# Kernel optimization log

Hardware: AMD Instinct MI355X
Metric: run time of the kernel (lower is better)

Reference implementation:

```python
import jax, jax.numpy as jnp
import numpy as np

H = 64  # hidden_size, hard-coded in module


def _lstm_layer(xs, W_ih, W_hh, b_ih, b_hh):
    """Run one LSTM layer over time-major xs [T, B, D_in].
    PyTorch gate order: i, f, g, o. Returns (hs [T,B,H], h_last [B,H])."""
    T, B, _ = xs.shape
    b = b_ih + b_hh
    # Precompute input contribution for all timesteps: [T, B, 4H]
    x_gates = jnp.einsum('tbd,gd->tbg', xs, W_ih) + b

    def step(carry, xg_t):
        h, c = carry
        gates = xg_t + h @ W_hh.T  # [B, 4H]
        i, f, g, o = jnp.split(gates, 4, axis=-1)
        i = jax.nn.sigmoid(i)
        f = jax.nn.sigmoid(f)
        g = jnp.tanh(g)
        o = jax.nn.sigmoid(o)
        c = f * c + i * g
        h = o * jnp.tanh(c)
        return (h, c), h

    h0 = jnp.zeros((B, H), xs.dtype)
    c0 = jnp.zeros((B, H), xs.dtype)
    (h_last, _), hs = jax.lax.scan(step, (h0, c0), x_gates)
    return hs, h_last


def setup_inputs() -> dict:
    key = jax.random.key(0)
    ks = jax.random.split(key, 12)
    B, T, C_in, E = 256, 4000, 1, 128
    s0 = 1.0 / np.sqrt(H)  # PyTorch LSTM init scale
    inp = {
        'x': jax.random.normal(ks[0], (B, T, C_in), jnp.float32),
        'W_ih0': jax.random.uniform(ks[1], (4 * H, C_in), jnp.float32, -s0, s0),
        'W_hh0': jax.random.uniform(ks[2], (4 * H, H), jnp.float32, -s0, s0),
        'b_ih0': jax.random.uniform(ks[3], (4 * H,), jnp.float32, -s0, s0),
        'b_hh0': jax.random.uniform(ks[4], (4 * H,), jnp.float32, -s0, s0),
        'W_ih1': jax.random.uniform(ks[5], (4 * H, H), jnp.float32, -s0, s0),
        'W_hh1': jax.random.uniform(ks[6], (4 * H, H), jnp.float32, -s0, s0),
        'b_ih1': jax.random.uniform(ks[7], (4 * H,), jnp.float32, -s0, s0),
        'b_hh1': jax.random.uniform(ks[8], (4 * H,), jnp.float32, -s0, s0),
        'W_fc': jax.random.uniform(ks[9], (E, H), jnp.float32, -s0, s0),
        'b_fc': jax.random.uniform(ks[10], (E,), jnp.float32, -s0, s0),
    }
    return inp


def reference(x, W_ih0, W_hh0, b_ih0, b_hh0, W_ih1, W_hh1, b_ih1, b_hh1, W_fc, b_fc):
    # x: [B, T, 1] (batch_first) -> time-major [T, B, 1]
    xs = jnp.swapaxes(x.astype(jnp.float32), 0, 1)
    hs0, _ = _lstm_layer(xs, W_ih0, W_hh0, b_ih0, b_hh0)
    _, h_last = _lstm_layer(hs0, W_ih1, W_hh1, b_ih1, b_hh1)
    # fc on final hidden state of the last layer: [B, E]
    return h_last @ W_fc.T + b_fc
```

## Files before the change

kernel.cpp:

```cpp
#include <hip/hip_runtime.h>

#define TT 4000
#define HH 64
#define NB 256
#define EE 128

typedef __attribute__((ext_vector_type(2))) _Float16 h2;
typedef __attribute__((ext_vector_type(8))) _Float16 h8;

__device__ __forceinline__ float ftanh(float x) {
    return fmaf(2.f, __builtin_amdgcn_rcpf(1.f + __expf(-2.f * x)), -1.f);
}

#if __has_builtin(__builtin_amdgcn_fdot2)
#define FDOT2(a, b, c) __builtin_amdgcn_fdot2((a), (b), (c), false)
#else
#define FDOT2(a, b, c) fmaf((float)(a).x, (float)(b).x, fmaf((float)(a).y, (float)(b).y, (c)))
#endif

#define H2V(V, i) (__builtin_shufflevector((V), (V), 2 * (i), 2 * (i) + 1))

template <int CTRL>
__device__ __forceinline__ float dpp_mov(float v) {
    return __int_as_float(__builtin_amdgcn_update_dpp(
        0, __float_as_int(v), CTRL, 0xF, 0xF, true));
}
#define DPP_XOR1 0xB1
#define DPP_XOR2 0x4E
#define DPP_FB   0x44
#define DPP_OB   0xEE
#define DPP_SHR4 0x114

#define CVT2(d0, d1, s) h2 d0 = h2{(_Float16)(s).x, (_Float16)(s).y}, \
                           d1 = h2{(_Float16)(s).z, (_Float16)(s).w};

#define D4(acc, W0, W1, W2, W3, Hv) \
    acc = FDOT2(W0, H2V(Hv, 0), acc); \
    acc = FDOT2(W1, H2V(Hv, 1), acc); \
    acc = FDOT2(W2, H2V(Hv, 2), acc); \
    acc = FDOT2(W3, H2V(Hv, 3), acc);

__global__ __launch_bounds__(256, 1)
void lstm2_fc_kernel(const float* __restrict__ x,
                     const float* __restrict__ W_ih0,
                     const float* __restrict__ W_hh0,
                     const float* __restrict__ b_ih0,
                     const float* __restrict__ b_hh0,
                     const float* __restrict__ W_ih1,
                     const float* __restrict__ W_hh1,
                     const float* __restrict__ b_ih1,
                     const float* __restrict__ b_hh1,
                     const float* __restrict__ W_fc,
                     const float* __restrict__ b_fc,
                     float* __restrict__ out)
{
    const int b    = blockIdx.x;
    const int tid  = threadIdx.x;
    const int w    = tid >> 6;
    const int lane = tid & 63;
    const int ss   = lane & 1;
    const int uu   = (lane >> 1) & 1;
    const int pp   = (lane >> 2) & 1;
    const int nn   = (lane >> 3) & 1;
    const int na   = w * 8 + (lane >> 4) * 2 + nn;
    const int nb   = na + 32;
    const int gidx = pp + 2 * uu;

    __shared__ float x_s[TT];
    __shared__ __align__(16) _Float16 hbuf[2][2 * HH];

    for (int t = tid; t < TT; t += 256) x_s[t] = x[(size_t)b * TT + t];
    if (tid < 4 * HH) ((_Float16*)hbuf)[tid] = (_Float16)0.f;

    const int rowa = gidx * HH + na;
    const int rowb = gidx * HH + nb;
    const float4* p0 = (const float4*)(W_hh0 + rowa * HH + ss * 32);
    const float4* p1 = (const float4*)(W_ih1 + rowa * HH + ss * 32);
    const float4* p2 = (const float4*)(W_hh1 + rowa * HH + ss * 32);
    const float4* p3 = (const float4*)(W_hh0 + rowb * HH + ss * 32);
    const float4* p4 = (const float4*)(W_ih1 + rowb * HH + ss * 32);
    const float4* p5 = (const float4*)(W_hh1 + rowb * HH + ss * 32);
    float4 qa0 = p0[0], qa1 = p0[1], qa2 = p0[2], qa3 = p0[3];
    float4 qa4 = p0[4], qa5 = p0[5], qa6 = p0[6], qa7 = p0[7];
    float4 qb0 = p1[0], qb1 = p1[1], qb2 = p1[2], qb3 = p1[3];
    float4 qb4 = p1[4], qb5 = p1[5], qb6 = p1[6], qb7 = p1[7];
    float4 qc0 = p2[0], qc1 = p2[1], qc2 = p2[2], qc3 = p2[3];
    float4 qc4 = p2[4], qc5 = p2[5], qc6 = p2[6], qc7 = p2[7];
    float4 qd0 = p3[0], qd1 = p3[1], qd2 = p3[2], qd3 = p3[3];
    float4 qd4 = p3[4], qd5 = p3[5], qd6 = p3[6], qd7 = p3[7];
    float4 qe0 = p4[0], qe1 = p4[1], qe2 = p4[2], qe3 = p4[3];
    float4 qe4 = p4[4], qe5 = p4[5], qe6 = p4[6], qe7 = p4[7];
    float4 qf0 = p5[0], qf1 = p5[1], qf2 = p5[2], qf3 = p5[3];
    float4 qf4 = p5[4], qf5 = p5[5], qf6 = p5[6], qf7 = p5[7];
    CVT2(A0,  A1,  qa0) CVT2(A2,  A3,  qa1) CVT2(A4,  A5,  qa2) CVT2(A6,  A7,  qa3)
    CVT2(A8,  A9,  qa4) CVT2(A10, A11, qa5) CVT2(A12, A13, qa6) CVT2(A14, A15, qa7)
    CVT2(B0,  B1,  qb0) CVT2(B2,  B3,  qb1) CVT2(B4,  B5,  qb2) CVT2(B6,  B7,  qb3)
    CVT2(B8,  B9,  qb4) CVT2(B10, B11, qb5) CVT2(B12, B13, qb6) CVT2(B14, B15, qb7)
    CVT2(C0,  C1,  qc0) CVT2(C2,  C3,  qc1) CVT2(C4,  C5,  qc2) CVT2(C6,  C7,  qc3)
    CVT2(C8,  C9,  qc4) CVT2(C10, C11, qc5) CVT2(C12, C13, qc6) CVT2(C14, C15, qc7)
    CVT2(D0,  D1,  qd0) CVT2(D2,  D3,  qd1) CVT2(D4,  D5,  qd2) CVT2(D6,  D7,  qd3)
    CVT2(D8,  D9,  qd4) CVT2(D10, D11, qd5) CVT2(D12, D13, qd6) CVT2(D14, D15, qd7)
    CVT2(E0,  E1,  qe0) CVT2(E2,  E3,  qe1) CVT2(E4,  E5,  qe2) CVT2(E6,  E7,  qe3)
    CVT2(E8,  E9,  qe4) CVT2(E10, E11, qe5) CVT2(E12, E13, qe6) CVT2(E14, E15, qe7)
    CVT2(F0,  F1,  qf0) CVT2(F2,  F3,  qf1) CVT2(F4,  F5,  qf2) CVT2(F6,  F7,  qf3)
    CVT2(F8,  F9,  qf4) CVT2(F10, F11, qf5) CVT2(F12, F13, qf6) CVT2(F14, F15, qf7)

    float wxa  = W_ih0[rowa];
    float wxb  = W_ih0[rowb];
    float bb0a = b_ih0[rowa] + b_hh0[rowa];
    float bb0b = b_ih0[rowb] + b_hh0[rowb];
    float bb1a = b_ih1[rowa] + b_hh1[rowa];
    float bb1b = b_ih1[rowb] + b_hh1[rowb];

    asm volatile("" : "+v"(A0), "+v"(A1), "+v"(A2),  "+v"(A3),
                      "+v"(A4), "+v"(A5), "+v"(A6),  "+v"(A7),
                      "+v"(A8), "+v"(A9), "+v"(A10), "+v"(A11),
                      "+v"(A12),"+v"(A13),"+v"(A14), "+v"(A15),
                      "+v"(B0), "+v"(B1), "+v"(B2),  "+v"(B3),
                      "+v"(B4), "+v"(B5), "+v"(B6),  "+v"(B7));
    asm volatile("" : "+v"(B8), "+v"(B9), "+v"(B10), "+v"(B11),
                      "+v"(B12),"+v"(B13),"+v"(B14), "+v"(B15),
                      "+v"(C0), "+v"(C1), "+v"(C2),  "+v"(C3),
                      "+v"(C4), "+v"(C5), "+v"(C6),  "+v"(C7),
                      "+v"(C8), "+v"(C9), "+v"(C10), "+v"(C11),
                      "+v"(C12),"+v"(C13),"+v"(C14), "+v"(C15));
    asm volatile("" : "+v"(D0), "+v"(D1), "+v"(D2),  "+v"(D3),
                      "+v"(D4), "+v"(D5), "+v"(D6),  "+v"(D7),
                      "+v"(D8), "+v"(D9), "+v"(D10), "+v"(D11),
                      "+v"(D12),"+v"(D13),"+v"(D14), "+v"(D15),
                      "+v"(E0), "+v"(E1), "+v"(E2),  "+v"(E3),
                      "+v"(E4), "+v"(E5), "+v"(E6),  "+v"(E7));
    asm volatile("" : "+v"(E8), "+v"(E9), "+v"(E10), "+v"(E11),
                      "+v"(E12),"+v"(E13),"+v"(E14), "+v"(E15),
                      "+v"(F0), "+v"(F1), "+v"(F2),  "+v"(F3),
                      "+v"(F4), "+v"(F5), "+v"(F6),  "+v"(F7),
                      "+v"(F8), "+v"(F9), "+v"(F10), "+v"(F11),
                      "+v"(F12),"+v"(F13),"+v"(F14), "+v"(F15));
    asm volatile("" : "+v"(wxa), "+v"(wxb), "+v"(bb0a),
                      "+v"(bb0b),"+v"(bb1a),"+v"(bb1b));

    const bool isg = (gidx == 2);
    const float kk = isg ? -2.f : -1.f;
    const float mm = isg ?  2.f :  1.f;
    const float aa = isg ? -1.f :  0.f;

    const bool wlane = (pp == 1) && (uu == 0);
    const int  hoffa = ss * HH + na;
    const int  hoffb = ss * HH + nb;
    float cca = 0.f, ccb = 0.f;

    __syncthreads();

    for (int t = 0; t <= TT; ++t) {
        const float xt = x_s[(t < TT) ? t : 0];
        const h8* hb = (const h8*)hbuf[t & 1];
        h8 Ha = hb[4 * ss + 0], Hc = hb[4 * ss + 1];
        h8 He = hb[4 * ss + 2], Hg = hb[4 * ss + 3];
        h8 Ga = hb[8 + 4 * ss + 0], Gc = hb[8 + 4 * ss + 1];
        h8 Ge = hb[8 + 4 * ss + 2], Gg = hb[8 + 4 * ss + 3];

        float acc0a = ss ? 0.f : fmaf(xt, wxa, bb0a);
        float acc0b = ss ? 0.f : fmaf(xt, wxb, bb0b);
        float acc1a = ss ? 0.f : bb1a;
        float acc1b = ss ? 0.f : bb1b;

        D4(acc0a, A0,  A1,  A2,  A3,  Ha)  D4(acc0b, D0,  D1,  D2,  D3,  Ha)
        D4(acc1a, B0,  B1,  B2,  B3,  Ha)  D4(acc1b, E0,  E1,  E2,  E3,  Ha)
        D4(acc0a, A4,  A5,  A6,  A7,  Hc)  D4(acc0b, D4,  D5,  D6,  D7,  Hc)
        D4(acc1a, B4,  B5,  B6,  B7,  Hc)  D4(acc1b, E4,  E5,  E6,  E7,  Hc)
        D4(acc0a, A8,  A9,  A10, A11, He)  D4(acc0b, D8,  D9,  D10, D11, He)
        D4(acc1a, B8,  B9,  B10, B11, He)  D4(acc1b, E8,  E9,  E10, E11, He)
        D4(acc0a, A12, A13, A14, A15, Hg)  D4(acc0b, D12, D13, D14, D15, Hg)
        D4(acc1a, B12, B13, B14, B15, Hg)  D4(acc1b, E12, E13, E14, E15, Hg)
        D4(acc1a, C0,  C1,  C2,  C3,  Ga)  D4(acc1b, F0,  F1,  F2,  F3,  Ga)
        D4(acc1a, C4,  C5,  C6,  C7,  Gc)  D4(acc1b, F4,  F5,  F6,  F7,  Gc)
        D4(acc1a, C8,  C9,  C10, C11, Ge)  D4(acc1b, F8,  F9,  F10, F11, Ge)
        D4(acc1a, C12, C13, C14, C15, Gg)  D4(acc1b, F12, F13, F14, F15, Gg)

        acc0a += dpp_mov<DPP_XOR1>(acc0a);
        acc0b += dpp_mov<DPP_XOR1>(acc0b);
        acc1a += dpp_mov<DPP_XOR1>(acc1a);
        acc1b += dpp_mov<DPP_XOR1>(acc1b);

        float za  = ss ? acc1a : acc0a;
        float zb  = ss ? acc1b : acc0b;
        float eza = __expf(kk * za);
        float ezb = __expf(kk * zb);
        float va  = fmaf(mm, __builtin_amdgcn_rcpf(1.f + eza), aa);
        float vb  = fmaf(mm, __builtin_amdgcn_rcpf(1.f + ezb), aa);

        float igqa = va * dpp_mov<DPP_XOR2>(va);
        float igqb = vb * dpp_mov<DPP_XOR2>(vb);
        float iga  = dpp_mov<DPP_SHR4>(igqa);
        float igb  = dpp_mov<DPP_SHR4>(igqb);
        float fba  = dpp_mov<DPP_FB>(va);
        float fbb  = dpp_mov<DPP_FB>(vb);
        float oba  = dpp_mov<DPP_OB>(va);
        float obb  = dpp_mov<DPP_OB>(vb);

        float cna = fmaf(fba, cca, iga);
        float cnb = fmaf(fbb, ccb, igb);
        float hna = oba * ftanh(cna);
        float hnb = obb * ftanh(cnb);
        bool ok = ss ? (t > 0) : (t < TT);
        cca = ok ? cna : cca;
        ccb = ok ? cnb : ccb;
        if (wlane && ok) {
            _Float16* hw = hbuf[(t + 1) & 1];
            hw[hoffa] = (_Float16)hna;
            hw[hoffb] = (_Float16)hnb;
        }

        __syncthreads();
    }

    if (tid < EE) {
        const _Float16* h1f = &hbuf[(TT + 1) & 1][HH];
        float acc = b_fc[tid];
        const float4* wf = (const float4*)(W_fc + tid * HH);
        #pragma unroll
        for (int k = 0; k < HH / 4; ++k) {
            float4 v = wf[k];
            acc = fmaf(v.x, (float)h1f[4*k+0], acc);
            acc = fmaf(v.y, (float)h1f[4*k+1], acc);
            acc = fmaf(v.z, (float)h1f[4*k+2], acc);
            acc = fmaf(v.w, (float)h1f[4*k+3], acc);
        }
        out[(size_t)b * EE + tid] = acc;
    }
}

extern "C" void kernel_launch(void* const* d_in, const int* in_sizes, int n_in,
                              void* d_out, int out_size, void* d_ws, size_t ws_size,
                              hipStream_t stream) {
    const float* x     = (const float*)d_in[0];
    const float* W_ih0 = (const float*)d_in[1];
    const float* W_hh0 = (const float*)d_in[2];
    const float* b_ih0 = (const float*)d_in[3];
    const float* b_hh0 = (const float*)d_in[4];
    const float* W_ih1 = (const float*)d_in[5];
    const float* W_hh1 = (const float*)d_in[6];
    const float* b_ih1 = (const float*)d_in[7];
    const float* b_hh1 = (const float*)d_in[8];
    const float* W_fc  = (const float*)d_in[9];
    const float* b_fc  = (const float*)d_in[10];
    float* out = (float*)d_out;

    lstm2_fc_kernel<<<dim3(NB), dim3(256), 0, stream>>>(
        x, W_ih0, W_hh0, b_ih0, b_hh0, W_ih1, W_hh1, b_ih1, b_hh1, W_fc, b_fc, out);
}
```

Before: 1.821 ms.

## Process two batch sequences per block to interleave independent recurrences

Each block now runs two batch elements' LSTM recurrences together, sharing the register-resident weights and interleaving their dot-product chains, DPP reductions and activations. The grid is halved to 128 blocks and the shared state buffers are doubled. The aim is to hide the serial per-step latency with independent work and to amortize one barrier per step across two sequences. The cost is that half the compute units go idle and register and LDS use per thread grows.

```diff
diff --git a/kernel.cpp b/kernel.cpp
--- a/kernel.cpp
+++ b/kernel.cpp
@@ -33,12 +33,6 @@
 
 #define CVT2(d0, d1, s) h2 d0 = h2{(_Float16)(s).x, (_Float16)(s).y}, \
                            d1 = h2{(_Float16)(s).z, (_Float16)(s).w};
-
-#define D4(acc, W0, W1, W2, W3, Hv) \
-    acc = FDOT2(W0, H2V(Hv, 0), acc); \
-    acc = FDOT2(W1, H2V(Hv, 1), acc); \
-    acc = FDOT2(W2, H2V(Hv, 2), acc); \
-    acc = FDOT2(W3, H2V(Hv, 3), acc);
 
 __global__ __launch_bounds__(256, 1)
 void lstm2_fc_kernel(const float* __restrict__ x,
@@ -66,11 +60,18 @@
     const int nb   = na + 32;
     const int gidx = pp + 2 * uu;
 
-    __shared__ float x_s[TT];
-    __shared__ __align__(16) _Float16 hbuf[2][2 * HH];
-
-    for (int t = tid; t < TT; t += 256) x_s[t] = x[(size_t)b * TT + t];
-    if (tid < 4 * HH) ((_Float16*)hbuf)[tid] = (_Float16)0.f;
+    __shared__ float x_s[2][TT];
+    __shared__ __align__(16) _Float16 hbuf[2][2][2 * HH];
+
+    for (int t = tid; t < TT; t += 256) {
+        x_s[0][t] = x[(size_t)(2 * b + 0) * TT + t];
+        x_s[1][t] = x[(size_t)(2 * b + 1) * TT + t];
+    }
+    {
+        _Float16* hz = (_Float16*)hbuf;
+        hz[tid] = (_Float16)0.f;
+        hz[tid + 256] = (_Float16)0.f;
+    }
 
     const int rowa = gidx * HH + na;
     const int rowb = gidx * HH + nb;
@@ -147,77 +148,162 @@
     const bool wlane = (pp == 1) && (uu == 0);
     const int  hoffa = ss * HH + na;
     const int  hoffb = ss * HH + nb;
-    float cca = 0.f, ccb = 0.f;
+    float ccaP = 0.f, ccbP = 0.f;
+    float ccaQ = 0.f, ccbQ = 0.f;
 
     __syncthreads();
 
+    #define ROWP(Aj, Dj, Bj, Ej, Cj, Fj, Hv, Gv, e) \
+        s0aP = FDOT2(Aj, H2V(Hv, e), s0aP); \
+        s0bP = FDOT2(Dj, H2V(Hv, e), s0bP); \
+        s1aP = FDOT2(Bj, H2V(Hv, e), s1aP); \
+        s1bP = FDOT2(Ej, H2V(Hv, e), s1bP); \
+        s2aP = FDOT2(Cj, H2V(Gv, e), s2aP); \
+        s2bP = FDOT2(Fj, H2V(Gv, e), s2bP);
+    #define ROWQ(Aj, Dj, Bj, Ej, Cj, Fj, Hv, Gv, e) \
+        s0aQ = FDOT2(Aj, H2V(Hv, e), s0aQ); \
+        s0bQ = FDOT2(Dj, H2V(Hv, e), s0bQ); \
+        s1aQ = FDOT2(Bj, H2V(Hv, e), s1aQ); \
+        s1bQ = FDOT2(Ej, H2V(Hv, e), s1bQ); \
+        s2aQ = FDOT2(Cj, H2V(Gv, e), s2aQ); \
+        s2bQ = FDOT2(Fj, H2V(Gv, e), s2bQ);
+
     for (int t = 0; t <= TT; ++t) {
-        const float xt = x_s[(t < TT) ? t : 0];
-        const h8* hb = (const h8*)hbuf[t & 1];
-        h8 Ha = hb[4 * ss + 0], Hc = hb[4 * ss + 1];
-        h8 He = hb[4 * ss + 2], Hg = hb[4 * ss + 3];
-        h8 Ga = hb[8 + 4 * ss + 0], Gc = hb[8 + 4 * ss + 1];
-        h8 Ge = hb[8 + 4 * ss + 2], Gg = hb[8 + 4 * ss + 3];
-
-        float acc0a = ss ? 0.f : fmaf(xt, wxa, bb0a);
-        float acc0b = ss ? 0.f : fmaf(xt, wxb, bb0b);
-        float acc1a = ss ? 0.f : bb1a;
-        float acc1b = ss ? 0.f : bb1b;
-
-        D4(acc0a, A0,  A1,  A2,  A3,  Ha)  D4(acc0b, D0,  D1,  D2,  D3,  Ha)
-        D4(acc1a, B0,  B1,  B2,  B3,  Ha)  D4(acc1b, E0,  E1,  E2,  E3,  Ha)
-        D4(acc0a, A4,  A5,  A6,  A7,  Hc)  D4(acc0b, D4,  D5,  D6,  D7,  Hc)
-        D4(acc1a, B4,  B5,  B6,  B7,  Hc)  D4(acc1b, E4,  E5,  E6,  E7,  Hc)
-        D4(acc0a, A8,  A9,  A10, A11, He)  D4(acc0b, D8,  D9,  D10, D11, He)
-        D4(acc1a, B8,  B9,  B10, B11, He)  D4(acc1b, E8,  E9,  E10, E11, He)
-        D4(acc0a, A12, A13, A14, A15, Hg)  D4(acc0b, D12, D13, D14, D15, Hg)
-        D4(acc1a, B12, B13, B14, B15, Hg)  D4(acc1b, E12, E13, E14, E15, Hg)
-        D4(acc1a, C0,  C1,  C2,  C3,  Ga)  D4(acc1b, F0,  F1,  F2,  F3,  Ga)
-        D4(acc1a, C4,  C5,  C6,  C7,  Gc)  D4(acc1b, F4,  F5,  F6,  F7,  Gc)
-        D4(acc1a, C8,  C9,  C10, C11, Ge)  D4(acc1b, F8,  F9,  F10, F11, Ge)
-        D4(acc1a, C12, C13, C14, C15, Gg)  D4(acc1b, F12, F13, F14, F15, Gg)
-
-        acc0a += dpp_mov<DPP_XOR1>(acc0a);
-        acc0b += dpp_mov<DPP_XOR1>(acc0b);
-        acc1a += dpp_mov<DPP_XOR1>(acc1a);
-        acc1b += dpp_mov<DPP_XOR1>(acc1b);
-
-        float za  = ss ? acc1a : acc0a;
-        float zb  = ss ? acc1b : acc0b;
-        float eza = __expf(kk * za);
-        float ezb = __expf(kk * zb);
-        float va  = fmaf(mm, __builtin_amdgcn_rcpf(1.f + eza), aa);
-        float vb  = fmaf(mm, __builtin_amdgcn_rcpf(1.f + ezb), aa);
-
-        float igqa = va * dpp_mov<DPP_XOR2>(va);
-        float igqb = vb * dpp_mov<DPP_XOR2>(vb);
-        float iga  = dpp_mov<DPP_SHR4>(igqa);
-        float igb  = dpp_mov<DPP_SHR4>(igqb);
-        float fba  = dpp_mov<DPP_FB>(va);
-        float fbb  = dpp_mov<DPP_FB>(vb);
-        float oba  = dpp_mov<DPP_OB>(va);
-        float obb  = dpp_mov<DPP_OB>(vb);
-
-        float cna = fmaf(fba, cca, iga);
-        float cnb = fmaf(fbb, ccb, igb);
-        float hna = oba * ftanh(cna);
-        float hnb = obb * ftanh(cnb);
+        const int tc = (t < TT) ? t : 0;
+        const float xtP = x_s[0][tc];
+        const float xtQ = x_s[1][tc];
+        const h8* hbP = (const h8*)hbuf[0][t & 1];
+        const h8* hbQ = (const h8*)hbuf[1][t & 1];
+        h8 HaP = hbP[4 * ss + 0], GaP = hbP[8 + 4 * ss + 0];
+        h8 HaQ = hbQ[4 * ss + 0], GaQ = hbQ[8 + 4 * ss + 0];
+        h8 HcP = hbP[4 * ss + 1], GcP = hbP[8 + 4 * ss + 1];
+        h8 HcQ = hbQ[4 * ss + 1], GcQ = hbQ[8 + 4 * ss + 1];
+        h8 HeP = hbP[4 * ss + 2], GeP = hbP[8 + 4 * ss + 2];
+        h8 HeQ = hbQ[4 * ss + 2], GeQ = hbQ[8 + 4 * ss + 2];
+        h8 HgP = hbP[4 * ss + 3], GgP = hbP[8 + 4 * ss + 3];
+        h8 HgQ = hbQ[4 * ss + 3], GgQ = hbQ[8 + 4 * ss + 3];
+
+        float s0aP = ss ? 0.f : fmaf(xtP, wxa, bb0a);
+        float s0bP = ss ? 0.f : fmaf(xtP, wxb, bb0b);
+        float s1aP = ss ? 0.f : bb1a;
+        float s1bP = ss ? 0.f : bb1b;
+        float s2aP = 0.f, s2bP = 0.f;
+        float s0aQ = ss ? 0.f : fmaf(xtQ, wxa, bb0a);
+        float s0bQ = ss ? 0.f : fmaf(xtQ, wxb, bb0b);
+        float s1aQ = ss ? 0.f : bb1a;
+        float s1bQ = ss ? 0.f : bb1b;
+        float s2aQ = 0.f, s2bQ = 0.f;
+
+        ROWP(A0,  D0,  B0,  E0,  C0,  F0,  HaP, GaP, 0)
+        ROWQ(A0,  D0,  B0,  E0,  C0,  F0,  HaQ, GaQ, 0)
+        ROWP(A1,  D1,  B1,  E1,  C1,  F1,  HaP, GaP, 1)
+        ROWQ(A1,  D1,  B1,  E1,  C1,  F1,  HaQ, GaQ, 1)
+        ROWP(A2,  D2,  B2,  E2,  C2,  F2,  HaP, GaP, 2)
+        ROWQ(A2,  D2,  B2,  E2,  C2,  F2,  HaQ, GaQ, 2)
+        ROWP(A3,  D3,  B3,  E3,  C3,  F3,  HaP, GaP, 3)
+        ROWQ(A3,  D3,  B3,  E3,  C3,  F3,  HaQ, GaQ, 3)
+        ROWP(A4,  D4,  B4,  E4,  C4,  F4,  HcP, GcP, 0)
+        ROWQ(A4,  D4,  B4,  E4,  C4,  F4,  HcQ, GcQ, 0)
+        ROWP(A5,  D5,  B5,  E5,  C5,  F5,  HcP, GcP, 1)
+        ROWQ(A5,  D5,  B5,  E5,  C5,  F5,  HcQ, GcQ, 1)
+        ROWP(A6,  D6,  B6,  E6,  C6,  F6,  HcP, GcP, 2)
+        ROWQ(A6,  D6,  B6,  E6,  C6,  F6,  HcQ, GcQ, 2)
+        ROWP(A7,  D7,  B7,  E7,  C7,  F7,  HcP, GcP, 3)
+        ROWQ(A7,  D7,  B7,  E7,  C7,  F7,  HcQ, GcQ, 3)
+        ROWP(A8,  D8,  B8,  E8,  C8,  F8,  HeP, GeP, 0)
+        ROWQ(A8,  D8,  B8,  E8,  C8,  F8,  HeQ, GeQ, 0)
+        ROWP(A9,  D9,  B9,  E9,  C9,  F9,  HeP, GeP, 1)
+        ROWQ(A9,  D9,  B9,  E9,  C9,  F9,  HeQ, GeQ, 1)
+        ROWP(A10, D10, B10, E10, C10, F10, HeP, GeP, 2)
+        ROWQ(A10, D10, B10, E10, C10, F10, HeQ, GeQ, 2)
+        ROWP(A11, D11, B11, E11, C11, F11, HeP, GeP, 3)
+        ROWQ(A11, D11, B11, E11, C11, F11, HeQ, GeQ, 3)
+        ROWP(A12, D12, B12, E12, C12, F12, HgP, GgP, 0)
+        ROWQ(A12, D12, B12, E12, C12, F12, HgQ, GgQ, 0)
+        ROWP(A13, D13, B13, E13, C13, F13, HgP, GgP, 1)
+        ROWQ(A13, D13, B13, E13, C13, F13, HgQ, GgQ, 1)
+        ROWP(A14, D14, B14, E14, C14, F14, HgP, GgP, 2)
+        ROWQ(A14, D14, B14, E14, C14, F14, HgQ, GgQ, 2)
+        ROWP(A15, D15, B15, E15, C15, F15, HgP, GgP, 3)
+        ROWQ(A15, D15, B15, E15, C15, F15, HgQ, GgQ, 3)
+
+        float acc0aP = s0aP,        acc0bP = s0bP;
+        float acc1aP = s1aP + s2aP, acc1bP = s1bP + s2bP;
+        float acc0aQ = s0aQ,        acc0bQ = s0bQ;
+        float acc1aQ = s1aQ + s2aQ, acc1bQ = s1bQ + s2bQ;
+
+        acc0aP += dpp_mov<DPP_XOR1>(acc0aP);
+        acc0bP += dpp_mov<DPP_XOR1>(acc0bP);
+        acc1aP += dpp_mov<DPP_XOR1>(acc1aP);
+        acc1bP += dpp_mov<DPP_XOR1>(acc1bP);
+        acc0aQ += dpp_mov<DPP_XOR1>(acc0aQ);
+        acc0bQ += dpp_mov<DPP_XOR1>(acc0bQ);
+        acc1aQ += dpp_mov<DPP_XOR1>(acc1aQ);
+        acc1bQ += dpp_mov<DPP_XOR1>(acc1bQ);
+
+        float zaP  = ss ? acc1aP : acc0aP;
+        float zbP  = ss ? acc1bP : acc0bP;
+        float zaQ  = ss ? acc1aQ : acc0aQ;
+        float zbQ  = ss ? acc1bQ : acc0bQ;
+        float ezaP = __expf(kk * zaP);
+        float ezbP = __expf(kk * zbP);
+        float ezaQ = __expf(kk * zaQ);
+        float ezbQ = __expf(kk * zbQ);
+        float vaP  = fmaf(mm, __builtin_amdgcn_rcpf(1.f + ezaP), aa);
+        float vbP  = fmaf(mm, __builtin_amdgcn_rcpf(1.f + ezbP), aa);
+        float vaQ  = fmaf(mm, __builtin_amdgcn_rcpf(1.f + ezaQ), aa);
+        float vbQ  = fmaf(mm, __builtin_amdgcn_rcpf(1.f + ezbQ), aa);
+
+        float igqaP = vaP * dpp_mov<DPP_XOR2>(vaP);
+        float igqbP = vbP * dpp_mov<DPP_XOR2>(vbP);
+        float igqaQ = vaQ * dpp_mov<DPP_XOR2>(vaQ);
+        float igqbQ = vbQ * dpp_mov<DPP_XOR2>(vbQ);
+        float igaP  = dpp_mov<DPP_SHR4>(igqaP);
+        float igbP  = dpp_mov<DPP_SHR4>(igqbP);
+        float igaQ  = dpp_mov<DPP_SHR4>(igqaQ);
+        float igbQ  = dpp_mov<DPP_SHR4>(igqbQ);
+        float fbaP  = dpp_mov<DPP_FB>(vaP);
+        float fbbP  = dpp_mov<DPP_FB>(vbP);
+        float fbaQ  = dpp_mov<DPP_FB>(vaQ);
+        float fbbQ  = dpp_mov<DPP_FB>(vbQ);
+        float obaP  = dpp_mov<DPP_OB>(vaP);
+        float obbP  = dpp_mov<DPP_OB>(vbP);
+        float obaQ  = dpp_mov<DPP_OB>(vaQ);
+        float obbQ  = dpp_mov<DPP_OB>(vbQ);
+
+        float cnaP = fmaf(fbaP, ccaP, igaP);
+        float cnbP = fmaf(fbbP, ccbP, igbP);
+        float cnaQ = fmaf(fbaQ, ccaQ, igaQ);
+        float cnbQ = fmaf(fbbQ, ccbQ, igbQ);
+        float hnaP = obaP * ftanh(cnaP);
+        float hnbP = obbP * ftanh(cnbP);
+        float hnaQ = obaQ * ftanh(cnaQ);
+        float hnbQ = obbQ * ftanh(cnbQ);
         bool ok = ss ? (t > 0) : (t < TT);
-        cca = ok ? cna : cca;
-        ccb = ok ? cnb : ccb;
+        ccaP = ok ? cnaP : ccaP;
+        ccbP = ok ? cnbP : ccbP;
+        ccaQ = ok ? cnaQ : ccaQ;
+        ccbQ = ok ? cnbQ : ccbQ;
         if (wlane && ok) {
-            _Float16* hw = hbuf[(t + 1) & 1];
-            hw[hoffa] = (_Float16)hna;
-            hw[hoffb] = (_Float16)hnb;
+            _Float16* hwP = hbuf[0][(t + 1) & 1];
+            _Float16* hwQ = hbuf[1][(t + 1) & 1];
+            hwP[hoffa] = (_Float16)hnaP;
+            hwP[hoffb] = (_Float16)hnbP;
+            hwQ[hoffa] = (_Float16)hnaQ;
+            hwQ[hoffb] = (_Float16)hnbQ;
         }
 
         __syncthreads();
     }
-
-    if (tid < EE) {
-        const _Float16* h1f = &hbuf[(TT + 1) & 1][HH];
-        float acc = b_fc[tid];
-        const float4* wf = (const float4*)(W_fc + tid * HH);
+    #undef ROWP
+    #undef ROWQ
+
+    {
+        const int e = tid >> 7;
+        const int j = tid & (EE - 1);
+        const _Float16* h1f = &hbuf[e][(TT + 1) & 1][HH];
+        float acc = b_fc[j];
+        const float4* wf = (const float4*)(W_fc + j * HH);
         #pragma unroll
         for (int k = 0; k < HH / 4; ++k) {
             float4 v = wf[k];
@@ -226,7 +312,7 @@
             acc = fmaf(v.z, (float)h1f[4*k+2], acc);
             acc = fmaf(v.w, (float)h1f[4*k+3], acc);
         }
-        out[(size_t)b * EE + tid] = acc;
+        out[(size_t)(2 * b + e) * EE + j] = acc;
     }
 }
 
@@ -246,6 +332,6 @@
     const float* b_fc  = (const float*)d_in[10];
     float* out = (float*)d_out;
 
-    lstm2_fc_kernel<<<dim3(NB), dim3(256), 0, stream>>>(
+    lstm2_fc_kernel<<<dim3(NB / 2), dim3(256), 0, stream>>>(
         x, W_ih0, W_hh0, b_ih0, b_hh0, W_ih1, W_hh1, b_ih1, b_hh1, W_fc, b_fc, out);
 }
```

Result: slower. 3.167 ms (+73.9%).
